# Kernel optimization log

Hardware: AMD Instinct MI355X
Metric: run time of the kernel (lower is better)

The kernel has to match this reference:

```python
import jax, jax.numpy as jnp
import numpy as np

B, N, D, H = 8, 1024, 512, 8
DH = D // H


def setup_inputs() -> dict:
    key = jax.random.key(0)
    ks = jax.random.split(key, 7)
    s = 1.0 / np.sqrt(D)
    return {
        "x": jax.random.normal(ks[0], (B, N, D), dtype=jnp.float32),
        "Wq": jax.random.normal(ks[1], (D, D), dtype=jnp.float32) * s,
        "bq": jax.random.normal(ks[2], (D,), dtype=jnp.float32) * 0.01,
        "Wk": jax.random.normal(ks[3], (D, D), dtype=jnp.float32) * s,
        "bk": jax.random.normal(ks[4], (D,), dtype=jnp.float32) * 0.01,
        "Wv": jax.random.normal(ks[5], (D, D), dtype=jnp.float32) * s,
        "bv": jax.random.normal(ks[6], (D,), dtype=jnp.float32) * 0.01,
    }


def reference(x, Wq, bq, Wk, bk, Wv, bv):
    # Q/K/V projections (nn.Linear: x @ W^T + b; here W stored as [in, out])
    q = x @ Wq + bq  # [B, N, D]
    k = x @ Wk + bk
    v = x @ Wv + bv
    # chunk(dim=2)+cat(dim=0) == split channels into H head groups
    q = q.reshape(B, N, H, DH)
    k = k.reshape(B, N, H, DH)
    v = v.reshape(B, N, H, DH)
    # NOTE: original applies NO 1/sqrt(head_dim) scaling
    scores = jnp.einsum("bqhd,bkhd->bhqk", q, k)  # [B, H, N, N]
    weights = jax.nn.softmax(scores, axis=-1)
    y = jnp.einsum("bhqk,bkhd->bqhd", weights, v)  # [B, N, H, DH]
    return y.reshape(B, N, D)
```

## Files before the change

kernel.cpp:

```cpp
#include <hip/hip_runtime.h>
#include <hip/hip_bf16.h>

typedef _Float16 half8 __attribute__((ext_vector_type(8)));
typedef _Float16 half4v __attribute__((ext_vector_type(4)));
typedef float floatx4 __attribute__((ext_vector_type(4)));

#define BB 8
#define NN 1024
#define DD 512
#define HH 8
#define DHH 64

__device__ __forceinline__ void gload_lds16(const _Float16* g, _Float16* l) {
    __builtin_amdgcn_global_load_lds(
        (const __attribute__((address_space(1))) void*)g,
        (__attribute__((address_space(3))) void*)l, 16, 0, 0);
}

__global__ __launch_bounds__(256) void cvt_kernel(const float* __restrict__ x,
                                                  const float* __restrict__ Wq,
                                                  const float* __restrict__ Wk,
                                                  const float* __restrict__ Wv,
                                                  _Float16* __restrict__ xh,
                                                  _Float16* __restrict__ Wt) {
    __shared__ __align__(16) _Float16 tb[64][72];
    int bx = blockIdx.x;
    int tid = threadIdx.x;
    if (bx < 4096) {
        int i = bx * 256 + tid;
        float4 v = ((const float4*)x)[i];
        half4v o;
        o[0] = (_Float16)v.x; o[1] = (_Float16)v.y;
        o[2] = (_Float16)v.z; o[3] = (_Float16)v.w;
        ((half4v*)xh)[i] = o;
        return;
    }
    int t = bx - 4096;
    int which = t >> 6;
    int rem = t & 63;
    int kt = (rem >> 3) * 64, nt = (rem & 7) * 64;
    const float* W = (which == 0) ? Wq : (which == 1) ? Wk : Wv;
    _Float16* Wto = Wt + (size_t)which * DD * DD;
    for (int i = 0; i < 16; i++) {
        int idx = tid + i * 256;
        int r = idx >> 6, c = idx & 63;
        tb[c][r] = (_Float16)W[(size_t)(kt + r) * DD + nt + c];
    }
    __syncthreads();
    for (int i = 0; i < 16; i++) {
        int idx = tid + i * 256;
        int r = idx >> 6, c = idx & 63;
        Wto[(size_t)(nt + r) * DD + kt + c] = tb[r][c];
    }
}

__global__ __launch_bounds__(256) void qkv_gemm_kernel(const _Float16* __restrict__ xh,
                                                       const _Float16* __restrict__ Wt,
                                                       const float* __restrict__ bq,
                                                       const float* __restrict__ bk,
                                                       const float* __restrict__ bv,
                                                       _Float16* __restrict__ QKV) {
    __shared__ __align__(16) _Float16 As[128 * 32];
    __shared__ __align__(16) _Float16 Bs[128 * 32];

    int which = blockIdx.z;
    const _Float16* Wtw = Wt + (size_t)which * DD * DD;
    const float* bias = (which == 0) ? bq : (which == 1) ? bk : bv;

    int tid = threadIdx.x;
    int wave = tid >> 6, lane = tid & 63;
    int quad = lane >> 4, l16 = lane & 15;
    int wm = wave >> 1, wn = wave & 1;
    int mBase = blockIdx.y * 128;
    int nBase = blockIdx.x * 128;

    int srow = wave * 32 + (lane >> 2);
    int scol = (lane & 3) * 8;
    const _Float16* ag = (which < 2)
        ? Wtw + (size_t)(nBase + srow) * DD + scol
        : xh  + (size_t)(mBase + srow) * DD + scol;
    const _Float16* bg = (which < 2)
        ? xh  + (size_t)(mBase + srow) * DD + scol
        : Wtw + (size_t)(nBase + srow) * DD + scol;
    _Float16* al = As + (wave * 32) * 32;
    _Float16* bl = Bs + (wave * 32) * 32;

    floatx4 acc[4][4];
    for (int i = 0; i < 4; i++)
        for (int j = 0; j < 4; j++) acc[i][j] = (floatx4){0.f, 0.f, 0.f, 0.f};

    for (int kk = 0; kk < DD; kk += 32) {
        __syncthreads();
        gload_lds16(ag + kk,            al);
        gload_lds16(ag + 16 * DD + kk,  al + 16 * 32);
        gload_lds16(bg + kk,            bl);
        gload_lds16(bg + 16 * DD + kk,  bl + 16 * 32);
        __syncthreads();

        half8 af[4], bf[4];
        for (int i = 0; i < 4; i++)
            af[i] = *(const half8*)&As[(wm * 64 + i * 16 + l16) * 32 + quad * 8];
        for (int j = 0; j < 4; j++)
            bf[j] = *(const half8*)&Bs[(wn * 64 + j * 16 + l16) * 32 + quad * 8];
        for (int i = 0; i < 4; i++)
            for (int j = 0; j < 4; j++)
                acc[i][j] = __builtin_amdgcn_mfma_f32_16x16x32_f16(af[i], bf[j], acc[i][j], 0, 0, 0);
    }

    if (which < 2) {
        _Float16* out = QKV + (size_t)which * (BB * NN) * DD;
        for (int i = 0; i < 4; i++) {
            int feat0 = nBase + wm * 64 + i * 16 + quad * 4;
            float4 b4 = *(const float4*)&bias[feat0];
            for (int j = 0; j < 4; j++) {
                int token = mBase + wn * 64 + j * 16 + l16;
                half4v pack;
                pack[0] = (_Float16)(acc[i][j][0] + b4.x);
                pack[1] = (_Float16)(acc[i][j][1] + b4.y);
                pack[2] = (_Float16)(acc[i][j][2] + b4.z);
                pack[3] = (_Float16)(acc[i][j][3] + b4.w);
                *(half4v*)&out[(size_t)token * DD + feat0] = pack;
            }
        }
    } else {
        _Float16* VT = QKV + (size_t)2 * (BB * NN) * DD;
        for (int j = 0; j < 4; j++) {
            int col = nBase + wn * 64 + j * 16 + l16;
            float bval = bias[col];
            for (int i = 0; i < 4; i++) {
                int row0 = mBase + wm * 64 + i * 16 + quad * 4;
                int b = row0 >> 10;
                int n = row0 & 1023;
                half4v pack;
                for (int reg = 0; reg < 4; reg++) pack[reg] = (_Float16)(acc[i][j][reg] + bval);
                *(half4v*)&VT[((size_t)b * 512 + col) * 1024 + n] = pack;
            }
        }
    }
}

__global__ __launch_bounds__(256) void attn_kernel(const _Float16* __restrict__ QKV,
                                                   float* __restrict__ out) {
    const _Float16* Q  = QKV;
    const _Float16* K  = QKV + (size_t)(BB * NN) * DD;
    const _Float16* VT = QKV + (size_t)2 * (BB * NN) * DD;

    __shared__ __align__(16) _Float16 Kt[128 * 64];
    __shared__ __align__(16) _Float16 Vt[64 * 128];
    __shared__ __align__(16) _Float16 PT[4][16 * 64];

    int tid = threadIdx.x;
    int wave = tid >> 6, lane = tid & 63;
    int quad = lane >> 4, l16 = lane & 15;
    int qt = blockIdx.x, h = blockIdx.y, b = blockIdx.z;

    const _Float16* Qb  = Q + ((size_t)b * NN) * DD + h * DHH;
    const _Float16* Kb  = K + ((size_t)b * NN) * DD + h * DHH;
    const _Float16* VTb = VT + ((size_t)b * 512 + h * 64) * 1024;

    int qrow = qt * 64 + wave * 16 + l16;
    half8 qf0 = *(const half8*)(Qb + (size_t)qrow * DD + 0 * 32 + quad * 8);
    half8 qf1 = *(const half8*)(Qb + (size_t)qrow * DD + 1 * 32 + quad * 8);

    floatx4 o[4];
    for (int nt = 0; nt < 4; nt++) o[nt] = (floatx4){0.f, 0.f, 0.f, 0.f};
    float m_i = -1e30f, l_i = 0.f;

    const _Float16* kg = Kb + (size_t)(wave * 32 + (lane >> 3)) * DD
                            + ((lane & 7) ^ (lane >> 3)) * 8;
    _Float16* kl = Kt + (wave * 32) * 64;
    _Float16* vl = Vt + (wave * 16) * 128;
    int l16sw = l16 & 7;

    for (int kt = 0; kt < 8; kt++) {
        __syncthreads();
        for (int i = 0; i < 4; i++)
            gload_lds16(kg + (size_t)(kt * 128 + i * 8) * DD, kl + (i * 8) * 64);
        for (int i = 0; i < 4; i++) {
            int vrow = wave * 16 + i * 4 + (lane >> 4);
            int vc = (lane & 15) ^ (i * 4 + (lane >> 4));
            gload_lds16(VTb + (size_t)vrow * 1024 + kt * 128 + vc * 8, vl + (i * 4) * 128);
        }
        __syncthreads();

        floatx4 s[8];
        for (int nt = 0; nt < 8; nt++) s[nt] = (floatx4){0.f, 0.f, 0.f, 0.f};
        for (int ks = 0; ks < 2; ks++) {
            half8 qf = ks ? qf1 : qf0;
            for (int nt = 0; nt < 8; nt++) {
                half8 kf = *(const half8*)&Kt[(nt * 16 + l16) * 64
                                              + (((ks * 4 + quad) ^ l16sw) * 8)];
                s[nt] = __builtin_amdgcn_mfma_f32_16x16x32_f16(kf, qf, s[nt], 0, 0, 0);
            }
        }

        float mx = -1e30f;
        for (int nt = 0; nt < 8; nt++)
            for (int r = 0; r < 4; r++) mx = fmaxf(mx, s[nt][r]);
        mx = fmaxf(mx, __shfl_xor(mx, 16, 64));
        mx = fmaxf(mx, __shfl_xor(mx, 32, 64));
        float mnew = fmaxf(m_i, mx);
        float alpha = __expf(m_i - mnew);
        m_i = mnew;
        float rs = 0.f;
        for (int nt = 0; nt < 8; nt++)
            for (int r = 0; r < 4; r++) {
                float p = __expf(s[nt][r] - mnew);
                s[nt][r] = p;
                rs += p;
            }
        rs += __shfl_xor(rs, 16, 64);
        rs += __shfl_xor(rs, 32, 64);
        l_i = l_i * alpha + rs;

        for (int nt = 0; nt < 4; nt++)
            for (int r = 0; r < 4; r++) o[nt][r] *= alpha;

        for (int hh = 0; hh < 2; hh++) {
            for (int ntl = 0; ntl < 4; ntl++) {
                floatx4 sv = s[hh * 4 + ntl];
                half4v p4;
                for (int r = 0; r < 4; r++) p4[r] = (_Float16)sv[r];
                *(half4v*)&PT[wave][l16 * 64 + (((2 * ntl + (quad >> 1)) ^ l16sw) * 8)
                               + (quad & 1) * 4] = p4;
            }
            for (int ks2h = 0; ks2h < 2; ks2h++) {
                half8 pf = *(const half8*)&PT[wave][l16 * 64
                                                   + (((ks2h * 4 + quad) ^ l16sw) * 8)];
                int ks2 = hh * 2 + ks2h;
                for (int nt = 0; nt < 4; nt++) {
                    half8 vf = *(const half8*)&Vt[(nt * 16 + l16) * 128
                                                  + (((ks2 * 4 + quad) ^ l16) * 8)];
                    o[nt] = __builtin_amdgcn_mfma_f32_16x16x32_f16(vf, pf, o[nt], 0, 0, 0);
                }
            }
        }
    }

    float inv = 1.0f / l_i;
    float* outb = out + ((size_t)b * NN) * DD + h * DHH;
    int row = qt * 64 + wave * 16 + l16;
    for (int nt = 0; nt < 4; nt++) {
        float4 st;
        st.x = o[nt][0] * inv; st.y = o[nt][1] * inv;
        st.z = o[nt][2] * inv; st.w = o[nt][3] * inv;
        *(float4*)&outb[(size_t)row * DD + nt * 16 + quad * 4] = st;
    }
}

extern "C" void kernel_launch(void* const* d_in, const int* in_sizes, int n_in,
                              void* d_out, int out_size, void* d_ws, size_t ws_size,
                              hipStream_t stream) {
    const float* x  = (const float*)d_in[0];
    const float* Wq = (const float*)d_in[1];
    const float* bq = (const float*)d_in[2];
    const float* Wk = (const float*)d_in[3];
    const float* bk = (const float*)d_in[4];
    const float* Wv = (const float*)d_in[5];
    const float* bv = (const float*)d_in[6];
    float* out = (float*)d_out;

    _Float16* xh  = (_Float16*)d_ws;
    _Float16* Wt  = xh + (size_t)(BB * NN) * DD;
    _Float16* QKV = Wt + (size_t)3 * DD * DD;

    hipLaunchKernelGGL(cvt_kernel, dim3(4096 + 192), dim3(256), 0, stream,
                       x, Wq, Wk, Wv, xh, Wt);
    hipLaunchKernelGGL(qkv_gemm_kernel, dim3(4, 64, 3), dim3(256), 0, stream,
                       xh, Wt, bq, bk, bv, QKV);
    hipLaunchKernelGGL(attn_kernel, dim3(16, 8, 8), dim3(256), 0, stream, QKV, out);
}
```

Measured before the change: 142.0 us.

## Read K/V fragments directly from global memory in attention, dropping LDS staging

The attention kernel no longer stages K and V tiles through shared memory with block-wide barriers. Each wave now loads its MFMA K and V fragments straight from global memory and relies on L1/L2 for reuse across the four waves. The grid is reordered so heads vary fastest, launch bounds request four blocks per CU, and the probability fp16 conversion uses packed round-toward-zero conversions. This removes the syncthreads and LDS traffic but adds redundant global loads per wave with less coalescing, and truncating conversion changes rounding slightly.

```diff
diff --git a/kernel.cpp b/kernel.cpp
--- a/kernel.cpp
+++ b/kernel.cpp
@@ -139,20 +139,18 @@
     }
 }
 
-__global__ __launch_bounds__(256) void attn_kernel(const _Float16* __restrict__ QKV,
-                                                   float* __restrict__ out) {
+__global__ __launch_bounds__(256, 4) void attn_kernel(const _Float16* __restrict__ QKV,
+                                                      float* __restrict__ out) {
     const _Float16* Q  = QKV;
     const _Float16* K  = QKV + (size_t)(BB * NN) * DD;
     const _Float16* VT = QKV + (size_t)2 * (BB * NN) * DD;
 
-    __shared__ __align__(16) _Float16 Kt[128 * 64];
-    __shared__ __align__(16) _Float16 Vt[64 * 128];
     __shared__ __align__(16) _Float16 PT[4][16 * 64];
 
     int tid = threadIdx.x;
     int wave = tid >> 6, lane = tid & 63;
     int quad = lane >> 4, l16 = lane & 15;
-    int qt = blockIdx.x, h = blockIdx.y, b = blockIdx.z;
+    int h = blockIdx.x, qt = blockIdx.y, b = blockIdx.z;
 
     const _Float16* Qb  = Q + ((size_t)b * NN) * DD + h * DHH;
     const _Float16* Kb  = K + ((size_t)b * NN) * DD + h * DHH;
@@ -166,30 +164,17 @@
     for (int nt = 0; nt < 4; nt++) o[nt] = (floatx4){0.f, 0.f, 0.f, 0.f};
     float m_i = -1e30f, l_i = 0.f;
 
-    const _Float16* kg = Kb + (size_t)(wave * 32 + (lane >> 3)) * DD
-                            + ((lane & 7) ^ (lane >> 3)) * 8;
-    _Float16* kl = Kt + (wave * 32) * 64;
-    _Float16* vl = Vt + (wave * 16) * 128;
+    const _Float16* kbase = Kb + (size_t)l16 * DD + quad * 8;
+    const _Float16* vbase = VTb + (size_t)l16 * 1024 + quad * 8;
     int l16sw = l16 & 7;
 
     for (int kt = 0; kt < 8; kt++) {
-        __syncthreads();
-        for (int i = 0; i < 4; i++)
-            gload_lds16(kg + (size_t)(kt * 128 + i * 8) * DD, kl + (i * 8) * 64);
-        for (int i = 0; i < 4; i++) {
-            int vrow = wave * 16 + i * 4 + (lane >> 4);
-            int vc = (lane & 15) ^ (i * 4 + (lane >> 4));
-            gload_lds16(VTb + (size_t)vrow * 1024 + kt * 128 + vc * 8, vl + (i * 4) * 128);
-        }
-        __syncthreads();
-
         floatx4 s[8];
         for (int nt = 0; nt < 8; nt++) s[nt] = (floatx4){0.f, 0.f, 0.f, 0.f};
         for (int ks = 0; ks < 2; ks++) {
             half8 qf = ks ? qf1 : qf0;
             for (int nt = 0; nt < 8; nt++) {
-                half8 kf = *(const half8*)&Kt[(nt * 16 + l16) * 64
-                                              + (((ks * 4 + quad) ^ l16sw) * 8)];
+                half8 kf = *(const half8*)(kbase + (size_t)(kt * 128 + nt * 16) * DD + ks * 32);
                 s[nt] = __builtin_amdgcn_mfma_f32_16x16x32_f16(kf, qf, s[nt], 0, 0, 0);
             }
         }
@@ -219,18 +204,18 @@
         for (int hh = 0; hh < 2; hh++) {
             for (int ntl = 0; ntl < 4; ntl++) {
                 floatx4 sv = s[hh * 4 + ntl];
-                half4v p4;
-                for (int r = 0; r < 4; r++) p4[r] = (_Float16)sv[r];
-                *(half4v*)&PT[wave][l16 * 64 + (((2 * ntl + (quad >> 1)) ^ l16sw) * 8)
-                               + (quad & 1) * 4] = p4;
+                int d0 = __builtin_bit_cast(int, __builtin_amdgcn_cvt_pkrtz(sv[0], sv[1]));
+                int d1 = __builtin_bit_cast(int, __builtin_amdgcn_cvt_pkrtz(sv[2], sv[3]));
+                *(int2*)&PT[wave][l16 * 64 + (((2 * ntl + (quad >> 1)) ^ l16sw) * 8)
+                               + (quad & 1) * 4] = make_int2(d0, d1);
             }
             for (int ks2h = 0; ks2h < 2; ks2h++) {
                 half8 pf = *(const half8*)&PT[wave][l16 * 64
                                                    + (((ks2h * 4 + quad) ^ l16sw) * 8)];
                 int ks2 = hh * 2 + ks2h;
                 for (int nt = 0; nt < 4; nt++) {
-                    half8 vf = *(const half8*)&Vt[(nt * 16 + l16) * 128
-                                                  + (((ks2 * 4 + quad) ^ l16) * 8)];
+                    half8 vf = *(const half8*)(vbase + (size_t)(nt * 16) * 1024
+                                               + kt * 128 + ks2 * 32);
                     o[nt] = __builtin_amdgcn_mfma_f32_16x16x32_f16(vf, pf, o[nt], 0, 0, 0);
                 }
             }
@@ -268,5 +253,5 @@
                        x, Wq, Wk, Wv, xh, Wt);
     hipLaunchKernelGGL(qkv_gemm_kernel, dim3(4, 64, 3), dim3(256), 0, stream,
                        xh, Wt, bq, bk, bv, QKV);
-    hipLaunchKernelGGL(attn_kernel, dim3(16, 8, 8), dim3(256), 0, stream, QKV, out);
-}
+    hipLaunchKernelGGL(attn_kernel, dim3(8, 16, 8), dim3(256), 0, stream, QKV, out);
+}
```

Result: slower. 220.3 us (+55.1%).
